# Kernel optimization log

Hardware: AMD Instinct MI355X
Metric: run time of the kernel (lower is better)

Reference implementation:

```python
import jax, jax.numpy as jnp
import numpy as np

N_NODES = 100000
HIDDEN = 128
N_CLASS = 10
N_EDGES = 1600000


def setup_inputs() -> dict:
    key = jax.random.key(0)
    ks = jax.random.split(key, 8)
    s = 1.0 / np.sqrt(HIDDEN)
    return {
        "edge_index": jax.random.randint(ks[0], (2, N_EDGES), 0, N_NODES, dtype=jnp.int32),
        "embedding": jax.random.normal(ks[1], (N_NODES, HIDDEN), jnp.float32),
        "W1": jax.random.normal(ks[2], (HIDDEN, HIDDEN), jnp.float32) * s,
        "b1": jnp.zeros((HIDDEN,), jnp.float32),
        "W2": jax.random.normal(ks[3], (HIDDEN, HIDDEN), jnp.float32) * s,
        "b2": jnp.zeros((HIDDEN,), jnp.float32),
        "W_out": jax.random.normal(ks[4], (HIDDEN, N_CLASS), jnp.float32) * s,
        "b_out": jnp.zeros((N_CLASS,), jnp.float32),
    }


def reference(edge_index, embedding, W1, b1, W2, b2, W_out, b_out):
    N = embedding.shape[0]
    # PyG GCNConv: add self-loops, symmetric normalization D^-1/2 (A+I) D^-1/2
    loops = jnp.arange(N, dtype=edge_index.dtype)
    src = jnp.concatenate([edge_index[0], loops])  # message sources
    dst = jnp.concatenate([edge_index[1], loops])  # aggregation targets
    deg = jax.ops.segment_sum(jnp.ones_like(dst, jnp.float32), dst, num_segments=N)
    inv_sqrt = jnp.where(deg > 0, jax.lax.rsqrt(jnp.maximum(deg, 1.0)), 0.0)
    norm = inv_sqrt[src] * inv_sqrt[dst]  # [E+N]

    x = embedding  # forward ignores input x, uses learned embedding table
    for W, b in ((W1, b1), (W2, b2)):
        h = x @ W                                      # [N, H]
        msg = h[src] * norm[:, None]                   # gather + scale, [E+N, H]
        agg = jax.ops.segment_sum(msg, dst, num_segments=N)
        x = jax.nn.relu(agg + b)
    return x @ W_out + b_out
```

## Files before the change

### kernel.cpp

```cpp
#include <hip/hip_runtime.h>
#include <hip/hip_bf16.h>

#define HID 128
#define NCLASS 10
#define PCHUNK 8192
#define HB 256

typedef unsigned int uint;
typedef unsigned short ushort;
typedef __attribute__((ext_vector_type(8))) __bf16 bf16x8;
typedef __attribute__((ext_vector_type(4))) float f32x4;

__device__ __forceinline__ uint bf16rne(float x) {
    uint u = __float_as_uint(x);
    return (u + 0x7FFFu + ((u >> 16) & 1u)) >> 16;
}
__device__ __forceinline__ uint pack2(float e0, float e1) {
    return bf16rne(e0) | (bf16rne(e1) << 16);
}
__device__ __forceinline__ void unpack2(uint w, float& lo, float& hi) {
    lo = __uint_as_float(w << 16);
    hi = __uint_as_float(w & 0xFFFF0000u);
}
__device__ __forceinline__ void split2(float e0, float e1, uint& h, uint& l) {
    uint h0 = bf16rne(e0), h1 = bf16rne(e1);
    float r0 = e0 - __uint_as_float(h0 << 16);
    float r1 = e1 - __uint_as_float(h1 << 16);
    h = h0 | (h1 << 16);
    l = bf16rne(r0) | (bf16rne(r1) << 16);
}
__device__ __forceinline__ bf16x8 as_bf16x8(uint4 u) {
    return __builtin_bit_cast(bf16x8, u);
}
__device__ __forceinline__ void unpack8(uint4 u, float* f) {
    unpack2(u.x, f[0], f[1]); unpack2(u.y, f[2], f[3]);
    unpack2(u.z, f[4], f[5]); unpack2(u.w, f[6], f[7]);
}

__global__ void pack_w_kernel(const float* __restrict__ W, uint* __restrict__ hi,
                              uint* __restrict__ lo) {
    const int s = blockIdx.x >> 3, t = blockIdx.x & 7, l = threadIdx.x;
    const int kb = s * 32 + (l >> 4) * 8, n = t * 16 + (l & 15);
    float f[8];
#pragma unroll
    for (int j = 0; j < 8; ++j) f[j] = W[(kb + j) * HID + n];
    uint4 h, lo4;
    split2(f[0], f[1], h.x, lo4.x);
    split2(f[2], f[3], h.y, lo4.y);
    split2(f[4], f[5], h.z, lo4.z);
    split2(f[6], f[7], h.w, lo4.w);
    const int fo = ((s * 8 + t) * 64 + l) * 4;
    *(uint4*)(hi + fo) = h;
    *(uint4*)(lo + fo) = lo4;
}

template <bool FP32IN>
__device__ __forceinline__ void gemm_body_mfma(
        const float* __restrict__ Xf,
        const uint* __restrict__ Xhi, const uint* __restrict__ Xlo,
        const uint* __restrict__ Wphi, const uint* __restrict__ Wplo,
        ushort* __restrict__ HS, int N, int bidx, int tid) {
    const int wv = tid >> 6;
    const int l = tid & 63;
    const int q = l >> 4;
    const int cm = l & 15;
    const long rowbase = (long)bidx * 128 + wv * 32;

    bf16x8 bhi[2][4], blo[2][4];
#pragma unroll
    for (int rt = 0; rt < 2; ++rt) {
        const long row = rowbase + rt * 16 + cm;
        const long rc = row < N ? row : (N - 1);
#pragma unroll
        for (int s = 0; s < 4; ++s) {
            if (FP32IN) {
                const float* xp = Xf + rc * HID + s * 32 + q * 8;
                const float4 a0 = ((const float4*)xp)[0];
                const float4 a1 = ((const float4*)xp)[1];
                uint4 h, lo4;
                split2(a0.x, a0.y, h.x, lo4.x);
                split2(a0.z, a0.w, h.y, lo4.y);
                split2(a1.x, a1.y, h.z, lo4.z);
                split2(a1.z, a1.w, h.w, lo4.w);
                bhi[rt][s] = as_bf16x8(h);
                blo[rt][s] = as_bf16x8(lo4);
            } else {
                const long o = rc * (HID / 2) + s * 16 + q * 4;
                bhi[rt][s] = as_bf16x8(*(const uint4*)(Xhi + o));
                blo[rt][s] = as_bf16x8(*(const uint4*)(Xlo + o));
            }
        }
    }

    f32x4 acc[2][8];
#pragma unroll
    for (int rt = 0; rt < 2; ++rt)
#pragma unroll
        for (int t = 0; t < 8; ++t) acc[rt][t] = (f32x4)0.0f;

#pragma unroll
    for (int s = 0; s < 4; ++s) {
#pragma unroll
        for (int t = 0; t < 8; ++t) {
            const int fo = ((s * 8 + t) * 64 + l) * 4;
            const bf16x8 whi = as_bf16x8(*(const uint4*)(Wphi + fo));
            const bf16x8 wlo = as_bf16x8(*(const uint4*)(Wplo + fo));
#pragma unroll
            for (int rt = 0; rt < 2; ++rt) {
                acc[rt][t] = __builtin_amdgcn_mfma_f32_16x16x32_bf16(whi, bhi[rt][s], acc[rt][t], 0, 0, 0);
                acc[rt][t] = __builtin_amdgcn_mfma_f32_16x16x32_bf16(whi, blo[rt][s], acc[rt][t], 0, 0, 0);
                acc[rt][t] = __builtin_amdgcn_mfma_f32_16x16x32_bf16(wlo, bhi[rt][s], acc[rt][t], 0, 0, 0);
            }
        }
    }

#pragma unroll
    for (int rt = 0; rt < 2; ++rt) {
        const long row = rowbase + rt * 16 + cm;
        if (row < N) {
#pragma unroll
            for (int t = 0; t < 8; ++t) {
                uint2 o;
                o.x = pack2(acc[rt][t][0], acc[rt][t][1]);
                o.y = pack2(acc[rt][t][2], acc[rt][t][3]);
                *(uint2*)&HS[row * HID + t * 16 + q * 4] = o;
            }
        }
    }
}

__global__ __launch_bounds__(256) void gemm1_hist_kernel(
        const float* __restrict__ emb, const uint* __restrict__ Wphi,
        const uint* __restrict__ Wplo, ushort* __restrict__ HS, int N,
        const int* __restrict__ dst, int* __restrict__ bcnt, int E, int GB, int NB) {
    __shared__ int h[400];
    if ((int)blockIdx.x < GB) {
        gemm_body_mfma<true>(emb, nullptr, nullptr, Wphi, Wplo, HS, N, blockIdx.x, threadIdx.x);
    } else {
        const int hb = blockIdx.x - GB;
        const int nblk = gridDim.x - GB;
        const int ech = (E + nblk - 1) / nblk;
        const int e0 = hb * ech;
        const int e1 = min(E, e0 + ech);
        for (int i = threadIdx.x; i < NB; i += 256) h[i] = 0;
        __syncthreads();
        for (int e = e0 + (int)threadIdx.x; e < e1; e += 256) atomicAdd(&h[dst[e] >> 8], 1);
        __syncthreads();
        for (int i = threadIdx.x; i < NB; i += 256)
            if (h[i]) atomicAdd(&bcnt[i], h[i]);
    }
}

__global__ __launch_bounds__(256) void gemm2_kernel(
        const uint* __restrict__ Xhi, const uint* __restrict__ Xlo,
        const uint* __restrict__ Wphi, const uint* __restrict__ Wplo,
        ushort* __restrict__ HS, int N) {
    gemm_body_mfma<false>(nullptr, Xhi, Xlo, Wphi, Wplo, HS, N, blockIdx.x, threadIdx.x);
}

__global__ __launch_bounds__(512) void scan_buckets_kernel(const int* __restrict__ bcnt,
                                                           int* bbase, int* gcursor, int NB, int E) {
    __shared__ int sh[512];
    const int t = threadIdx.x;
    const int v = (t < NB) ? bcnt[t] : 0;
    sh[t] = v;
    __syncthreads();
    for (int off = 1; off < 512; off <<= 1) {
        int x = (t >= off) ? sh[t - off] : 0;
        __syncthreads();
        sh[t] += x;
        __syncthreads();
    }
    const int excl = sh[t] - v;
    if (t < NB) { bbase[t] = excl; gcursor[t] = excl; }
    if (t == NB - 1) bbase[NB] = excl + v;
}

__global__ __launch_bounds__(256) void partition_kernel(
        const int* __restrict__ src, const int* __restrict__ dst,
        int* __restrict__ gcursor, uint* __restrict__ staged, int E, int NB) {
    __shared__ int hist[400], lbase[400], loff[400];
    const int t = threadIdx.x;
    const int e0 = blockIdx.x * PCHUNK;
    for (int i = t; i < NB; i += 256) { hist[i] = 0; loff[i] = 0; }
    __syncthreads();
#pragma unroll
    for (int j = 0; j < PCHUNK / 256; ++j) {
        const int e = e0 + j * 256 + t;
        if (e < E) atomicAdd(&hist[dst[e] >> 8], 1);
    }
    __syncthreads();
    for (int b = t; b < NB; b += 256)
        if (hist[b] > 0) lbase[b] = atomicAdd(&gcursor[b], hist[b]);
    __syncthreads();
#pragma unroll
    for (int j = 0; j < PCHUNK / 256; ++j) {
        const int e = e0 + j * 256 + t;
        if (e < E) {
            const int d = dst[e];
            const int b = d >> 8;
            const int pos = lbase[b] + atomicAdd(&loff[b], 1);
            staged[pos] = (uint)src[e] | ((uint)(d & 255) << 17);
        }
    }
}

__global__ __launch_bounds__(256) void fill_bucket_kernel(
        const uint* __restrict__ staged, const int* __restrict__ bbase,
        int* __restrict__ rps, int* __restrict__ deg, float* __restrict__ invs,
        int* __restrict__ col, int N) {
    __shared__ int h[256], cur[256], sh[256];
    const int b = blockIdx.x, t = threadIdx.x;
    const int w0 = bbase[b], w1 = bbase[b + 1];
    const int base0 = b << 8;
    h[t] = 0;
    __syncthreads();
    for (int i = w0 + t; i < w1; i += 256) atomicAdd(&h[staged[i] >> 17], 1);
    __syncthreads();
    const int my = h[t];
    sh[t] = my;
    __syncthreads();
    for (int off = 1; off < 256; off <<= 1) {
        int x = (t >= off) ? sh[t - off] : 0;
        __syncthreads();
        sh[t] += x;
        __syncthreads();
    }
    const int start = w0 + sh[t] - my;
    cur[t] = start;
    const int node = base0 + t;
    if (node < N) {
        deg[node] = my;
        rps[node] = start;
        invs[node] = rsqrtf((float)my + 1.0f);
    }
    __syncthreads();
    for (int i = w0 + t; i < w1; i += 256) {
        const uint u = staged[i];
        const int p = atomicAdd(&cur[u >> 17], 1);
        col[p] = (int)(u & 0x1FFFFu);
    }
}

__global__ __launch_bounds__(256) void pull_relu_kernel(
        const int* __restrict__ rps, const int* __restrict__ deg, const int* __restrict__ col,
        const uint* __restrict__ HS, const float* __restrict__ invs,
        const float* __restrict__ b, uint* __restrict__ Xhi, uint* __restrict__ Xlo, int N) {
    const int g = blockIdx.x * 256 + threadIdx.x;
    const int node = g >> 3;
    if (node >= N) return;
    const int lane = g & 7;
    const int d = deg[node];
    const int p = rps[node];
    const uint4* H4 = (const uint4*)HS;
    const size_t so = (size_t)node * 16 + lane * 2;

    float acc[16];
    {
        const float sn = invs[node];
        float f[16];
        unpack8(H4[so], f);
        unpack8(H4[so + 1], f + 8);
#pragma unroll
        for (int j = 0; j < 16; ++j) acc[j] = f[j] * sn;
    }
    int i = 0;
    for (; i + 4 <= d; i += 4) {
        const int s0 = col[p + i], s1 = col[p + i + 1], s2 = col[p + i + 2], s3 = col[p + i + 3];
        const float w0 = invs[s0], w1 = invs[s1], w2 = invs[s2], w3 = invs[s3];
        const uint4 a0 = H4[(size_t)s0 * 16 + lane * 2], a0b = H4[(size_t)s0 * 16 + lane * 2 + 1];
        const uint4 a1 = H4[(size_t)s1 * 16 + lane * 2], a1b = H4[(size_t)s1 * 16 + lane * 2 + 1];
        const uint4 a2 = H4[(size_t)s2 * 16 + lane * 2], a2b = H4[(size_t)s2 * 16 + lane * 2 + 1];
        const uint4 a3 = H4[(size_t)s3 * 16 + lane * 2], a3b = H4[(size_t)s3 * 16 + lane * 2 + 1];
        float f[16];
        unpack8(a0, f); unpack8(a0b, f + 8);
#pragma unroll
        for (int j = 0; j < 16; ++j) acc[j] += f[j] * w0;
        unpack8(a1, f); unpack8(a1b, f + 8);
#pragma unroll
        for (int j = 0; j < 16; ++j) acc[j] += f[j] * w1;
        unpack8(a2, f); unpack8(a2b, f + 8);
#pragma unroll
        for (int j = 0; j < 16; ++j) acc[j] += f[j] * w2;
        unpack8(a3, f); unpack8(a3b, f + 8);
#pragma unroll
        for (int j = 0; j < 16; ++j) acc[j] += f[j] * w3;
    }
    for (; i < d; ++i) {
        const int s0 = col[p + i];
        const float w0 = invs[s0];
        const uint4 a0 = H4[(size_t)s0 * 16 + lane * 2], a0b = H4[(size_t)s0 * 16 + lane * 2 + 1];
        float f[16];
        unpack8(a0, f); unpack8(a0b, f + 8);
#pragma unroll
        for (int j = 0; j < 16; ++j) acc[j] += f[j] * w0;
    }
    const float sn = invs[node];
    float x[16];
#pragma unroll
    for (int j = 0; j < 16; ++j)
        x[j] = sn * fmaxf(acc[j] * sn + b[lane * 16 + j], 0.0f);
    uint4 h0, l0, h1, l1;
    split2(x[0], x[1], h0.x, l0.x);   split2(x[2], x[3], h0.y, l0.y);
    split2(x[4], x[5], h0.z, l0.z);   split2(x[6], x[7], h0.w, l0.w);
    split2(x[8], x[9], h1.x, l1.x);   split2(x[10], x[11], h1.y, l1.y);
    split2(x[12], x[13], h1.z, l1.z); split2(x[14], x[15], h1.w, l1.w);
    uint* oh = Xhi + (size_t)node * 64 + lane * 8;
    uint* ol = Xlo + (size_t)node * 64 + lane * 8;
    *(uint4*)oh = h0; *(uint4*)(oh + 4) = h1;
    *(uint4*)ol = l0; *(uint4*)(ol + 4) = l1;
}

__global__ __launch_bounds__(256) void pull_out_kernel(
        const int* __restrict__ rps, const int* __restrict__ deg, const int* __restrict__ col,
        const uint* __restrict__ HS, const float* __restrict__ invs,
        const float* __restrict__ b2, const float* __restrict__ Wout,
        const float* __restrict__ bout, float* __restrict__ OUT, int N) {
    __shared__ float Wd[320 * 4];
    for (int t = threadIdx.x; t < 320; t += 256) {
        const int c = t >> 5, rem = t & 31, j4 = rem >> 3, l = rem & 7;
        const int k0 = l * 16 + j4 * 4;
        float4 w;
        w.x = Wout[(k0 + 0) * NCLASS + c];
        w.y = Wout[(k0 + 1) * NCLASS + c];
        w.z = Wout[(k0 + 2) * NCLASS + c];
        w.w = Wout[(k0 + 3) * NCLASS + c];
        ((float4*)Wd)[t] = w;
    }
    __syncthreads();

    const int g = blockIdx.x * 256 + threadIdx.x;
    const int node = g >> 3;
    if (node >= N) return;
    const int lane = g & 7;
    const int d = deg[node];
    const int p = rps[node];
    const uint4* H4 = (const uint4*)HS;
    const size_t so = (size_t)node * 16 + lane * 2;

    float acc[16];
    {
        float f[16];
        unpack8(H4[so], f);
        unpack8(H4[so + 1], f + 8);
#pragma unroll
        for (int j = 0; j < 16; ++j) acc[j] = f[j];
    }
    int i = 0;
    for (; i + 4 <= d; i += 4) {
        const int s0 = col[p + i], s1 = col[p + i + 1], s2 = col[p + i + 2], s3 = col[p + i + 3];
        const uint4 a0 = H4[(size_t)s0 * 16 + lane * 2], a0b = H4[(size_t)s0 * 16 + lane * 2 + 1];
        const uint4 a1 = H4[(size_t)s1 * 16 + lane * 2], a1b = H4[(size_t)s1 * 16 + lane * 2 + 1];
        const uint4 a2 = H4[(size_t)s2 * 16 + lane * 2], a2b = H4[(size_t)s2 * 16 + lane * 2 + 1];
        const uint4 a3 = H4[(size_t)s3 * 16 + lane * 2], a3b = H4[(size_t)s3 * 16 + lane * 2 + 1];
        float f[16];
        unpack8(a0, f); unpack8(a0b, f + 8);
#pragma unroll
        for (int j = 0; j < 16; ++j) acc[j] += f[j];
        unpack8(a1, f); unpack8(a1b, f + 8);
#pragma unroll
        for (int j = 0; j < 16; ++j) acc[j] += f[j];
        unpack8(a2, f); unpack8(a2b, f + 8);
#pragma unroll
        for (int j = 0; j < 16; ++j) acc[j] += f[j];
        unpack8(a3, f); unpack8(a3b, f + 8);
#pragma unroll
        for (int j = 0; j < 16; ++j) acc[j] += f[j];
    }
    for (; i < d; ++i) {
        const int s0 = col[p + i];
        const uint4 a0 = H4[(size_t)s0 * 16 + lane * 2], a0b = H4[(size_t)s0 * 16 + lane * 2 + 1];
        float f[16];
        unpack8(a0, f); unpack8(a0b, f + 8);
#pragma unroll
        for (int j = 0; j < 16; ++j) acc[j] += f[j];
    }
    const float sn = invs[node];
    float x[16];
#pragma unroll
    for (int j = 0; j < 16; ++j) x[j] = fmaxf(acc[j] * sn + b2[lane * 16 + j], 0.0f);

    const float4 xv0 = make_float4(x[0], x[1], x[2], x[3]);
    const float4 xv1 = make_float4(x[4], x[5], x[6], x[7]);
    const float4 xv2 = make_float4(x[8], x[9], x[10], x[11]);
    const float4 xv3 = make_float4(x[12], x[13], x[14], x[15]);
    const float4* Wd4 = (const float4*)Wd;
#pragma unroll
    for (int c = 0; c < NCLASS; ++c) {
        const float4* wp = Wd4 + c * 32 + lane;
        const float4 w0 = wp[0], w1 = wp[8], w2 = wp[16], w3 = wp[24];
        float s = xv0.x * w0.x + xv0.y * w0.y + xv0.z * w0.z + xv0.w * w0.w
                + xv1.x * w1.x + xv1.y * w1.y + xv1.z * w1.z + xv1.w * w1.w
                + xv2.x * w2.x + xv2.y * w2.y + xv2.z * w2.z + xv2.w * w2.w
                + xv3.x * w3.x + xv3.y * w3.y + xv3.z * w3.z + xv3.w * w3.w;
        s += __shfl_xor(s, 1, 8);
        s += __shfl_xor(s, 2, 8);
        s += __shfl_xor(s, 4, 8);
        if (lane == (c & 7)) OUT[(size_t)node * NCLASS + c] = s + bout[c];
    }
}

extern "C" void kernel_launch(void* const* d_in, const int* in_sizes, int n_in,
                              void* d_out, int out_size, void* d_ws, size_t ws_size,
                              hipStream_t stream) {
    const int* ei     = (const int*)d_in[0];
    const float* emb  = (const float*)d_in[1];
    const float* W1   = (const float*)d_in[2];
    const float* b1   = (const float*)d_in[3];
    const float* W2   = (const float*)d_in[4];
    const float* b2   = (const float*)d_in[5];
    const float* Wout = (const float*)d_in[6];
    const float* bout = (const float*)d_in[7];
    float* out        = (float*)d_out;

    const int E = in_sizes[0] / 2;
    const int N = in_sizes[1] / HID;
    const int* src = ei;
    const int* dst = ei + E;
    (void)ws_size; (void)n_in; (void)out_size;

    const int GB = (N + 127) / 128;
    const int NB = (N + 255) >> 8;
    const int PB = (E + PCHUNK - 1) / PCHUNK;

    char* ws = (char*)d_ws;
    size_t off = 0;
    auto alloc = [&](size_t bytes) {
        void* p = ws + off;
        off = (off + bytes + 4095) & ~(size_t)4095;
        return p;
    };
    int*   bcnt    = (int*)alloc(512 * 4);
    int*   bbase   = (int*)alloc(512 * 4);
    int*   gcursor = (int*)alloc(512 * 4);
    int*   deg     = (int*)alloc((size_t)N * 4);
    int*   rps     = (int*)alloc((size_t)N * 4);
    float* invs    = (float*)alloc((size_t)N * 4);
    int*   col     = (int*)alloc((size_t)E * 4);
    uint*  staged  = (uint*)alloc((size_t)E * 4);
    uint*  Wp1hi   = (uint*)alloc(HID * HID * 2);
    uint*  Wp1lo   = (uint*)alloc(HID * HID * 2);
    uint*  Wp2hi   = (uint*)alloc(HID * HID * 2);
    uint*  Wp2lo   = (uint*)alloc(HID * HID * 2);
    uint*  HS      = (uint*)alloc((size_t)N * HID * 2);
    uint*  X1hi    = (uint*)alloc((size_t)N * HID * 2);
    uint*  X1lo    = (uint*)alloc((size_t)N * HID * 2);

    pack_w_kernel<<<32, 64, 0, stream>>>(W1, Wp1hi, Wp1lo);
    pack_w_kernel<<<32, 64, 0, stream>>>(W2, Wp2hi, Wp2lo);

    hipMemsetAsync(bcnt, 0, 512 * 4, stream);
    gemm1_hist_kernel<<<GB + HB, 256, 0, stream>>>(emb, Wp1hi, Wp1lo, (ushort*)HS, N,
                                                   dst, bcnt, E, GB, NB);
    scan_buckets_kernel<<<1, 512, 0, stream>>>(bcnt, bbase, gcursor, NB, E);
    partition_kernel<<<PB, 256, 0, stream>>>(src, dst, gcursor, staged, E, NB);
    fill_bucket_kernel<<<NB, 256, 0, stream>>>(staged, bbase, rps, deg, invs, col, N);

    pull_relu_kernel<<<(N * 8 + 255) / 256, 256, 0, stream>>>(
        rps, deg, col, HS, invs, b1, X1hi, X1lo, N);

    gemm2_kernel<<<GB, 256, 0, stream>>>(X1hi, X1lo, Wp2hi, Wp2lo, (ushort*)HS, N);
    pull_out_kernel<<<(N * 8 + 255) / 256, 256, 0, stream>>>(
        rps, deg, col, HS, invs, b2, Wout, bout, out, N);
}
```

Measured before the change: 357.9 us.

## Fuse weight packing into histogram, overlap gemm1 with partition, drop X1 low part

Weight packing now runs in the same launch as the destination histogram, and the first GEMM runs alongside edge partitioning instead of alongside the histogram. That removes two small launches and rebalances which work overlaps. The intermediate activation is kept only as a single bf16 array, with no lo residual, so the second GEMM uses two MFMAs per tile instead of three and skips an N×128 bf16 read and write. Degree is derived from consecutive row pointers instead of a separate array. The price is lower precision in the second layer's input.

```diff
diff --git a/kernel.cpp b/kernel.cpp
--- a/kernel.cpp
+++ b/kernel.cpp
@@ -37,9 +37,10 @@
     unpack2(u.z, f[4], f[5]); unpack2(u.w, f[6], f[7]);
 }
 
-__global__ void pack_w_kernel(const float* __restrict__ W, uint* __restrict__ hi,
-                              uint* __restrict__ lo) {
-    const int s = blockIdx.x >> 3, t = blockIdx.x & 7, l = threadIdx.x;
+__device__ __forceinline__ void pack_w_body(const float* __restrict__ W,
+                                            uint* __restrict__ hi, uint* __restrict__ lo,
+                                            int slot, int l) {
+    const int s = slot >> 3, t = slot & 7;
     const int kb = s * 32 + (l >> 4) * 8, n = t * 16 + (l & 15);
     float f[8];
 #pragma unroll
@@ -49,15 +50,39 @@
     split2(f[2], f[3], h.y, lo4.y);
     split2(f[4], f[5], h.z, lo4.z);
     split2(f[6], f[7], h.w, lo4.w);
-    const int fo = ((s * 8 + t) * 64 + l) * 4;
+    const int fo = (slot * 64 + l) * 4;
     *(uint4*)(hi + fo) = h;
     *(uint4*)(lo + fo) = lo4;
 }
 
+__global__ __launch_bounds__(256) void hist_pack_kernel(
+        const int* __restrict__ dst, int* __restrict__ bcnt, int E, int NB,
+        const float* __restrict__ W1, uint* __restrict__ W1hi, uint* __restrict__ W1lo,
+        const float* __restrict__ W2, uint* __restrict__ W2hi, uint* __restrict__ W2lo) {
+    __shared__ int h[400];
+    const int t = threadIdx.x;
+    if ((int)blockIdx.x < HB) {
+        const int ech = (E + HB - 1) / HB;
+        const int e0 = blockIdx.x * ech;
+        const int e1 = min(E, e0 + ech);
+        for (int i = t; i < NB; i += 256) h[i] = 0;
+        __syncthreads();
+        for (int e = e0 + t; e < e1; e += 256) atomicAdd(&h[dst[e] >> 8], 1);
+        __syncthreads();
+        for (int i = t; i < NB; i += 256)
+            if (h[i]) atomicAdd(&bcnt[i], h[i]);
+    } else {
+        const int pb = blockIdx.x - HB;
+        const int slot = (pb & 7) * 4 + (t >> 6);
+        const int l = t & 63;
+        if (pb < 8) pack_w_body(W1, W1hi, W1lo, slot, l);
+        else        pack_w_body(W2, W2hi, W2lo, slot, l);
+    }
+}
+
 template <bool FP32IN>
 __device__ __forceinline__ void gemm_body_mfma(
-        const float* __restrict__ Xf,
-        const uint* __restrict__ Xhi, const uint* __restrict__ Xlo,
+        const float* __restrict__ Xf, const uint* __restrict__ Xhi,
         const uint* __restrict__ Wphi, const uint* __restrict__ Wplo,
         ushort* __restrict__ HS, int N, int bidx, int tid) {
     const int wv = tid >> 6;
@@ -87,7 +112,6 @@
             } else {
                 const long o = rc * (HID / 2) + s * 16 + q * 4;
                 bhi[rt][s] = as_bf16x8(*(const uint4*)(Xhi + o));
-                blo[rt][s] = as_bf16x8(*(const uint4*)(Xlo + o));
             }
         }
     }
@@ -108,7 +132,8 @@
 #pragma unroll
             for (int rt = 0; rt < 2; ++rt) {
                 acc[rt][t] = __builtin_amdgcn_mfma_f32_16x16x32_bf16(whi, bhi[rt][s], acc[rt][t], 0, 0, 0);
-                acc[rt][t] = __builtin_amdgcn_mfma_f32_16x16x32_bf16(whi, blo[rt][s], acc[rt][t], 0, 0, 0);
+                if (FP32IN)
+                    acc[rt][t] = __builtin_amdgcn_mfma_f32_16x16x32_bf16(whi, blo[rt][s], acc[rt][t], 0, 0, 0);
                 acc[rt][t] = __builtin_amdgcn_mfma_f32_16x16x32_bf16(wlo, bhi[rt][s], acc[rt][t], 0, 0, 0);
             }
         }
@@ -129,58 +154,17 @@
     }
 }
 
-__global__ __launch_bounds__(256) void gemm1_hist_kernel(
+__global__ __launch_bounds__(256) void gemm1_part_kernel(
         const float* __restrict__ emb, const uint* __restrict__ Wphi,
         const uint* __restrict__ Wplo, ushort* __restrict__ HS, int N,
-        const int* __restrict__ dst, int* __restrict__ bcnt, int E, int GB, int NB) {
-    __shared__ int h[400];
-    if ((int)blockIdx.x < GB) {
-        gemm_body_mfma<true>(emb, nullptr, nullptr, Wphi, Wplo, HS, N, blockIdx.x, threadIdx.x);
-    } else {
-        const int hb = blockIdx.x - GB;
-        const int nblk = gridDim.x - GB;
-        const int ech = (E + nblk - 1) / nblk;
-        const int e0 = hb * ech;
-        const int e1 = min(E, e0 + ech);
-        for (int i = threadIdx.x; i < NB; i += 256) h[i] = 0;
-        __syncthreads();
-        for (int e = e0 + (int)threadIdx.x; e < e1; e += 256) atomicAdd(&h[dst[e] >> 8], 1);
-        __syncthreads();
-        for (int i = threadIdx.x; i < NB; i += 256)
-            if (h[i]) atomicAdd(&bcnt[i], h[i]);
-    }
-}
-
-__global__ __launch_bounds__(256) void gemm2_kernel(
-        const uint* __restrict__ Xhi, const uint* __restrict__ Xlo,
-        const uint* __restrict__ Wphi, const uint* __restrict__ Wplo,
-        ushort* __restrict__ HS, int N) {
-    gemm_body_mfma<false>(nullptr, Xhi, Xlo, Wphi, Wplo, HS, N, blockIdx.x, threadIdx.x);
-}
-
-__global__ __launch_bounds__(512) void scan_buckets_kernel(const int* __restrict__ bcnt,
-                                                           int* bbase, int* gcursor, int NB, int E) {
-    __shared__ int sh[512];
-    const int t = threadIdx.x;
-    const int v = (t < NB) ? bcnt[t] : 0;
-    sh[t] = v;
-    __syncthreads();
-    for (int off = 1; off < 512; off <<= 1) {
-        int x = (t >= off) ? sh[t - off] : 0;
-        __syncthreads();
-        sh[t] += x;
-        __syncthreads();
-    }
-    const int excl = sh[t] - v;
-    if (t < NB) { bbase[t] = excl; gcursor[t] = excl; }
-    if (t == NB - 1) bbase[NB] = excl + v;
-}
-
-__global__ __launch_bounds__(256) void partition_kernel(
         const int* __restrict__ src, const int* __restrict__ dst,
-        int* __restrict__ gcursor, uint* __restrict__ staged, int E, int NB) {
+        int* __restrict__ gcursor, uint* __restrict__ staged, int E, int PB, int NB) {
     __shared__ int hist[400], lbase[400], loff[400];
     const int t = threadIdx.x;
+    if ((int)blockIdx.x >= PB) {
+        gemm_body_mfma<true>(emb, nullptr, Wphi, Wplo, HS, N, blockIdx.x - PB, t);
+        return;
+    }
     const int e0 = blockIdx.x * PCHUNK;
     for (int i = t; i < NB; i += 256) { hist[i] = 0; loff[i] = 0; }
     __syncthreads();
@@ -205,10 +189,35 @@
     }
 }
 
+__global__ __launch_bounds__(256) void gemm2_kernel(
+        const uint* __restrict__ Xhi, const uint* __restrict__ Wphi,
+        const uint* __restrict__ Wplo, ushort* __restrict__ HS, int N) {
+    gemm_body_mfma<false>(nullptr, Xhi, Wphi, Wplo, HS, N, blockIdx.x, threadIdx.x);
+}
+
+__global__ __launch_bounds__(512) void scan_buckets_kernel(const int* __restrict__ bcnt,
+                                                           int* bbase, int* gcursor,
+                                                           int* rps, int NB, int E, int N) {
+    __shared__ int sh[512];
+    const int t = threadIdx.x;
+    const int v = (t < NB) ? bcnt[t] : 0;
+    sh[t] = v;
+    __syncthreads();
+    for (int off = 1; off < 512; off <<= 1) {
+        int x = (t >= off) ? sh[t - off] : 0;
+        __syncthreads();
+        sh[t] += x;
+        __syncthreads();
+    }
+    const int excl = sh[t] - v;
+    if (t < NB) { bbase[t] = excl; gcursor[t] = excl; }
+    if (t == NB - 1) bbase[NB] = excl + v;
+    if (t == 0) rps[N] = E;
+}
+
 __global__ __launch_bounds__(256) void fill_bucket_kernel(
         const uint* __restrict__ staged, const int* __restrict__ bbase,
-        int* __restrict__ rps, int* __restrict__ deg, float* __restrict__ invs,
-        int* __restrict__ col, int N) {
+        int* __restrict__ rps, float* __restrict__ invs, int* __restrict__ col, int N) {
     __shared__ int h[256], cur[256], sh[256];
     const int b = blockIdx.x, t = threadIdx.x;
     const int w0 = bbase[b], w1 = bbase[b + 1];
@@ -230,7 +239,6 @@
     cur[t] = start;
     const int node = base0 + t;
     if (node < N) {
-        deg[node] = my;
         rps[node] = start;
         invs[node] = rsqrtf((float)my + 1.0f);
     }
@@ -243,15 +251,15 @@
 }
 
 __global__ __launch_bounds__(256) void pull_relu_kernel(
-        const int* __restrict__ rps, const int* __restrict__ deg, const int* __restrict__ col,
+        const int* __restrict__ rps, const int* __restrict__ col,
         const uint* __restrict__ HS, const float* __restrict__ invs,
-        const float* __restrict__ b, uint* __restrict__ Xhi, uint* __restrict__ Xlo, int N) {
+        const float* __restrict__ b, uint* __restrict__ Xhi, int N) {
     const int g = blockIdx.x * 256 + threadIdx.x;
     const int node = g >> 3;
     if (node >= N) return;
     const int lane = g & 7;
-    const int d = deg[node];
     const int p = rps[node];
+    const int d = rps[node + 1] - p;
     const uint4* H4 = (const uint4*)HS;
     const size_t so = (size_t)node * 16 + lane * 2;
 
@@ -300,19 +308,17 @@
 #pragma unroll
     for (int j = 0; j < 16; ++j)
         x[j] = sn * fmaxf(acc[j] * sn + b[lane * 16 + j], 0.0f);
-    uint4 h0, l0, h1, l1;
-    split2(x[0], x[1], h0.x, l0.x);   split2(x[2], x[3], h0.y, l0.y);
-    split2(x[4], x[5], h0.z, l0.z);   split2(x[6], x[7], h0.w, l0.w);
-    split2(x[8], x[9], h1.x, l1.x);   split2(x[10], x[11], h1.y, l1.y);
-    split2(x[12], x[13], h1.z, l1.z); split2(x[14], x[15], h1.w, l1.w);
+    uint4 h0, h1;
+    h0.x = pack2(x[0], x[1]);   h0.y = pack2(x[2], x[3]);
+    h0.z = pack2(x[4], x[5]);   h0.w = pack2(x[6], x[7]);
+    h1.x = pack2(x[8], x[9]);   h1.y = pack2(x[10], x[11]);
+    h1.z = pack2(x[12], x[13]); h1.w = pack2(x[14], x[15]);
     uint* oh = Xhi + (size_t)node * 64 + lane * 8;
-    uint* ol = Xlo + (size_t)node * 64 + lane * 8;
     *(uint4*)oh = h0; *(uint4*)(oh + 4) = h1;
-    *(uint4*)ol = l0; *(uint4*)(ol + 4) = l1;
 }
 
 __global__ __launch_bounds__(256) void pull_out_kernel(
-        const int* __restrict__ rps, const int* __restrict__ deg, const int* __restrict__ col,
+        const int* __restrict__ rps, const int* __restrict__ col,
         const uint* __restrict__ HS, const float* __restrict__ invs,
         const float* __restrict__ b2, const float* __restrict__ Wout,
         const float* __restrict__ bout, float* __restrict__ OUT, int N) {
@@ -333,8 +339,8 @@
     const int node = g >> 3;
     if (node >= N) return;
     const int lane = g & 7;
-    const int d = deg[node];
     const int p = rps[node];
+    const int d = rps[node + 1] - p;
     const uint4* H4 = (const uint4*)HS;
     const size_t so = (size_t)node * 16 + lane * 2;
 
@@ -433,8 +439,7 @@
     int*   bcnt    = (int*)alloc(512 * 4);
     int*   bbase   = (int*)alloc(512 * 4);
     int*   gcursor = (int*)alloc(512 * 4);
-    int*   deg     = (int*)alloc((size_t)N * 4);
-    int*   rps     = (int*)alloc((size_t)N * 4);
+    int*   rps     = (int*)alloc((size_t)(N + 1) * 4);
     float* invs    = (float*)alloc((size_t)N * 4);
     int*   col     = (int*)alloc((size_t)E * 4);
     uint*  staged  = (uint*)alloc((size_t)E * 4);
@@ -444,22 +449,19 @@
     uint*  Wp2lo   = (uint*)alloc(HID * HID * 2);
     uint*  HS      = (uint*)alloc((size_t)N * HID * 2);
     uint*  X1hi    = (uint*)alloc((size_t)N * HID * 2);
-    uint*  X1lo    = (uint*)alloc((size_t)N * HID * 2);
-
-    pack_w_kernel<<<32, 64, 0, stream>>>(W1, Wp1hi, Wp1lo);
-    pack_w_kernel<<<32, 64, 0, stream>>>(W2, Wp2hi, Wp2lo);
 
     hipMemsetAsync(bcnt, 0, 512 * 4, stream);
-    gemm1_hist_kernel<<<GB + HB, 256, 0, stream>>>(emb, Wp1hi, Wp1lo, (ushort*)HS, N,
-                                                   dst, bcnt, E, GB, NB);
-    scan_buckets_kernel<<<1, 512, 0, stream>>>(bcnt, bbase, gcursor, NB, E);
-    partition_kernel<<<PB, 256, 0, stream>>>(src, dst, gcursor, staged, E, NB);
-    fill_bucket_kernel<<<NB, 256, 0, stream>>>(staged, bbase, rps, deg, invs, col, N);
+    hist_pack_kernel<<<HB + 16, 256, 0, stream>>>(dst, bcnt, E, NB,
+                                                  W1, Wp1hi, Wp1lo, W2, Wp2hi, Wp2lo);
+    scan_buckets_kernel<<<1, 512, 0, stream>>>(bcnt, bbase, gcursor, rps, NB, E, N);
+    gemm1_part_kernel<<<PB + GB, 256, 0, stream>>>(emb, Wp1hi, Wp1lo, (ushort*)HS, N,
+                                                   src, dst, gcursor, staged, E, PB, NB);
+    fill_bucket_kernel<<<NB, 256, 0, stream>>>(staged, bbase, rps, invs, col, N);
 
     pull_relu_kernel<<<(N * 8 + 255) / 256, 256, 0, stream>>>(
-        rps, deg, col, HS, invs, b1, X1hi, X1lo, N);
-
-    gemm2_kernel<<<GB, 256, 0, stream>>>(X1hi, X1lo, Wp2hi, Wp2lo, (ushort*)HS, N);
+        rps, col, HS, invs, b1, X1hi, N);
+
+    gemm2_kernel<<<GB, 256, 0, stream>>>(X1hi, Wp2hi, Wp2lo, (ushort*)HS, N);
     pull_out_kernel<<<(N * 8 + 255) / 256, 256, 0, stream>>>(
-        rps, deg, col, HS, invs, b2, Wout, bout, out, N);
-}
+        rps, col, HS, invs, b2, Wout, bout, out, N);
+}
```

New measurement: 337.0 us. 5.8% less time.
